# Kernel tuning notes

Measured on AMD Instinct MI355X. Metric: run time of the kernel, lower is better.

## Reference

```python
import jax, jax.numpy as jnp
import numpy as np

EMBED_DIM = 1024
NUM_HEADS = 16
HEAD_DIM = EMBED_DIM // NUM_HEADS
SCALE = HEAD_DIM ** -0.5
B, S = 2, 2048


def setup_inputs() -> dict:
    key = jax.random.key(0)
    ks = jax.random.split(key, 11)
    lim = 1.0 / np.sqrt(EMBED_DIM)
    def lin(kw, kb):
        W = jax.random.uniform(kw, (EMBED_DIM, EMBED_DIM), jnp.float32, -lim, lim)
        b = jax.random.uniform(kb, (EMBED_DIM,), jnp.float32, -lim, lim)
        return W, b
    Wq, bq = lin(ks[0], ks[1])
    Wk, bk = lin(ks[2], ks[3])
    Wv, bv = lin(ks[4], ks[5])
    Wo, bo = lin(ks[6], ks[7])
    query = jax.random.normal(ks[8], (B, S, EMBED_DIM), jnp.float32)
    key_t = jax.random.normal(ks[9], (B, S, EMBED_DIM), jnp.float32)
    value = jax.random.normal(ks[10], (B, S, EMBED_DIM), jnp.float32)
    return {"query": query, "key": key_t, "value": value,
            "Wq": Wq, "bq": bq, "Wk": Wk, "bk": bk,
            "Wv": Wv, "bv": bv, "Wo": Wo, "bo": bo}


def reference(query, key, value, Wq, bq, Wk, bk, Wv, bv, Wo, bo):
    # 'flash' path with attn_mask=None == full softmax attention (chunking is
    # only an execution schedule; per-chunk softmax is over the full key axis).
    b, s, _ = query.shape
    def heads(x, W, bias):
        y = x @ W.T + bias                      # [b, s, E]
        return y.reshape(b, s, NUM_HEADS, HEAD_DIM).transpose(0, 2, 1, 3)  # [b, h, s, d]
    q = heads(query, Wq, bq)
    k = heads(key, Wk, bk)
    v = heads(value, Wv, bv)
    scores = jnp.einsum('bhqd,bhkd->bhqk', q, k) * SCALE
    attn = jax.nn.softmax(scores, axis=-1)
    out = jnp.einsum('bhqk,bhkd->bhqd', attn, v)
    out = out.transpose(0, 2, 1, 3).reshape(b, s, EMBED_DIM)
    return out @ Wo.T + bo
```

## Files before the change

kernel.cpp:

```cpp
#include <hip/hip_runtime.h>

typedef unsigned short u16;
typedef unsigned int u32;
typedef __attribute__((ext_vector_type(8))) __bf16 bf16x8;
typedef __attribute__((ext_vector_type(4))) float f32x4;
typedef __attribute__((ext_vector_type(4))) unsigned short u16x4;
typedef __attribute__((ext_vector_type(8))) unsigned short u16x8;
typedef __attribute__((ext_vector_type(4))) unsigned int u32x4;

#define DEV static __device__ __forceinline__

DEV void async_copy16(const void* g, void* l) {
  __builtin_amdgcn_global_load_lds((const __attribute__((address_space(1))) void*)g,
                                   (__attribute__((address_space(3))) void*)l, 16, 0, 0);
}
DEV float b2f(u16 s) { union { unsigned u; float f; } v; v.u = ((unsigned)s) << 16; return v.f; }
DEV u16 f2b(float f) {
  union { float f; unsigned u; } v; v.f = f;
  unsigned r = v.u + 0x7FFFu + ((v.u >> 16) & 1u);
  return (u16)(r >> 16);
}
DEV u32 pack2bf(float a, float b) {
  u32 ua = __float_as_uint(a) + 0x8000u;
  u32 ub = __float_as_uint(b) + 0x8000u;
  return __builtin_amdgcn_perm(ub, ua, 0x07060302u);
}

#define MFMA(a, b, c) __builtin_amdgcn_mfma_f32_16x16x32_bf16((a), (b), (c), 0, 0, 0)

__global__ void detect_dtype(const unsigned* __restrict__ q, int* __restrict__ flag) {
  const int lane = threadIdx.x;
  const unsigned w = q[lane];
  const unsigned e = (w >> 7) & 0xFFu;
  const bool inr = (e >= 100u && e <= 132u);
  const unsigned long long m = __ballot(inr);
  if (lane == 0) flag[0] = (__popcll(m) >= 48) ? 1 : 0;
}

__global__ void convert_inputs(
    const void* s0, const void* s1, const void* s2,
    const void* s3, const void* s4, const void* s5, const void* s6,
    const void* s7, const void* s8, const void* s9, const void* s10,
    u16* __restrict__ d0, u16* __restrict__ d1, u16* __restrict__ d2,
    u16* __restrict__ d3, u16* __restrict__ d4, u16* __restrict__ d5, u16* __restrict__ d6,
    float* __restrict__ e7, float* __restrict__ e8, float* __restrict__ e9, float* __restrict__ e10,
    const int* __restrict__ flag)
{
  const int bi = blockIdx.y;
  const void* src = nullptr; u16* db = nullptr; float* df = nullptr; int n = 0;
  switch (bi) {
    case 0:  src = s0;  db = d0; n = 4194304; break;
    case 1:  src = s1;  db = d1; n = 4194304; break;
    case 2:  src = s2;  db = d2; n = 4194304; break;
    case 3:  src = s3;  db = d3; n = 1048576; break;
    case 4:  src = s4;  db = d4; n = 1048576; break;
    case 5:  src = s5;  db = d5; n = 1048576; break;
    case 6:  src = s6;  db = d6; n = 1048576; break;
    case 7:  src = s7;  df = e7; n = 1024; break;
    case 8:  src = s8;  df = e8; n = 1024; break;
    case 9:  src = s9;  df = e9; n = 1024; break;
    default: src = s10; df = e10; n = 1024; break;
  }
  const int isbf = flag[0];
  const int stride = gridDim.x * 256 * 8;
  for (int i = (blockIdx.x * 256 + threadIdx.x) * 8; i < n; i += stride) {
    if (db) {
      u16x8 v;
      if (isbf) {
        v = *(const u16x8*)((const u16*)src + i);
      } else {
        const float* sf = (const float*)src;
#pragma unroll
        for (int j = 0; j < 8; ++j) v[j] = f2b(sf[i + j]);
      }
      *(u16x8*)(db + i) = v;
    } else {
#pragma unroll
      for (int j = 0; j < 8; ++j) {
        float x = isbf ? b2f(((const u16*)src)[i + j]) : ((const float*)src)[i + j];
        df[i + j] = x;
      }
    }
  }
}

__global__ void gemm_qkv(const u16* __restrict__ X0, const u16* __restrict__ X1, const u16* __restrict__ X2,
                         const u16* __restrict__ W0, const u16* __restrict__ W1, const u16* __restrict__ W2,
                         const float* __restrict__ B0, const float* __restrict__ B1, const float* __restrict__ B2,
                         u16* __restrict__ Y0, u16* __restrict__ Y1, u16* __restrict__ Y2,
                         float* __restrict__ Yf, const int* __restrict__ flag, int mode0)
{
  __shared__ __align__(16) u16 smem[17408];
  u16* As = smem;
  u16* Bs = smem + 4096;

  const int z = blockIdx.z;
  const u16* X  = (z == 0) ? X0 : ((z == 1) ? X1 : X2);
  const u16* W  = (z == 0) ? W0 : ((z == 1) ? W1 : W2);
  const float* Bi = (z == 0) ? B0 : ((z == 1) ? B1 : B2);
  u16* Y        = (z == 0) ? Y0 : ((z == 1) ? Y1 : Y2);
  const int mode = mode0 ? mode0 : z;
  const int outbf = flag[0];

  const int t = threadIdx.x, wave = t >> 6, lane = t & 63;
  const int lane15 = lane & 15, quad = lane >> 4;
  const int m0 = blockIdx.y * 128, n0 = blockIdx.x * 128;

  const u16* gA = X + (size_t)(m0 + wave * 16 + (lane >> 2)) * 1024 + (lane & 3) * 8;
  const u16* gB = W + (size_t)(n0 + wave * 16 + (lane >> 2)) * 1024 + (lane & 3) * 8;
  u16* lA = &As[wave * 16 * 32];
  u16* lB = &Bs[wave * 16 * 32];

  f32x4 acc[4][4];
#pragma unroll
  for (int i = 0; i < 4; ++i)
#pragma unroll
    for (int j = 0; j < 4; ++j) acc[i][j] = (f32x4){0.f, 0.f, 0.f, 0.f};

  const int wr = wave >> 1, wc = wave & 1;

  for (int k0 = 0; k0 < 1024; k0 += 32) {
    async_copy16(gA, lA);
    async_copy16(gA + 64 * 1024, lA + 64 * 32);
    async_copy16(gB, lB);
    async_copy16(gB + 64 * 1024, lB + 64 * 32);
    gA += 32; gB += 32;
    __syncthreads();

    bf16x8 af[4], bfv[4];
#pragma unroll
    for (int mt = 0; mt < 4; ++mt)
      af[mt] = *(const bf16x8*)&As[(wr * 64 + mt * 16 + lane15) * 32 + quad * 8];
#pragma unroll
    for (int nt = 0; nt < 4; ++nt)
      bfv[nt] = *(const bf16x8*)&Bs[(wc * 64 + nt * 16 + lane15) * 32 + quad * 8];
#pragma unroll
    for (int mt = 0; mt < 4; ++mt)
#pragma unroll
      for (int nt = 0; nt < 4; ++nt)
        acc[mt][nt] = MFMA(af[mt], bfv[nt], acc[mt][nt]);
    __syncthreads();
  }

  const float qscale = 0.125f * 1.44269504088896340736f;

  if (mode == 2) {
    u16* T2 = smem;
    __syncthreads();
#pragma unroll
    for (int mt = 0; mt < 4; ++mt) {
      const int sl_base = wr * 64 + mt * 16 + quad * 4;
#pragma unroll
      for (int nt = 0; nt < 4; ++nt) {
        const int nn = wc * 64 + nt * 16 + lane15;
        const float bias_v = Bi[n0 + nn];
#pragma unroll
        for (int r = 0; r < 4; ++r) {
          const int sl = sl_base + r;
          const int sp = ((sl & 15) << 3) | (sl >> 4);
          T2[nn * 136 + sp] = f2b(acc[mt][nt][r] + bias_v);
        }
      }
    }
    __syncthreads();
    const size_t grow0 = (size_t)(m0 >> 11) * 1024 + n0;
    const int col0 = m0 & 2047;
#pragma unroll
    for (int i = 0; i < 8; ++i) {
      const int id = i * 256 + t;
      const int row = id >> 4, ch = id & 15;
      *(u16x8*)&Y[(grow0 + row) * 2048 + col0 + ch * 8] = *(const u16x8*)&T2[row * 136 + ch * 8];
    }
    return;
  }

#pragma unroll
  for (int mt = 0; mt < 4; ++mt) {
    const int m_base = m0 + wr * 64 + mt * 16 + quad * 4;
#pragma unroll
    for (int nt = 0; nt < 4; ++nt) {
      const int n = n0 + wc * 64 + nt * 16 + lane15;
      const float bias_v = Bi[n];
#pragma unroll
      for (int r = 0; r < 4; ++r) {
        const int m = m_base + r;
        float v = acc[mt][nt][r] + bias_v;
        if (mode == 0) v *= qscale;
        if (mode == 3) {
          if (outbf) Y[(size_t)m * 1024 + n] = f2b(v);
          else       Yf[(size_t)m * 1024 + n] = v;
        } else {
          size_t addr = (((size_t)(m >> 11) * 16 + (n >> 6)) * 2048 + (size_t)(m & 2047)) * 64 + (n & 63);
          Y[addr] = f2b(v);
        }
      }
    }
  }
}

__global__ __launch_bounds__(256, 2) void flash_attn(const u16* __restrict__ Qs, const u16* __restrict__ Ks,
                                                     const u16* __restrict__ Vt, u16* __restrict__ AO)
{
  __shared__ __align__(16) u16 smem[32768];
  u16* Kt = smem;
  u16* Vs = smem + 8192;

  const int t = threadIdx.x, wave = t >> 6, lane = t & 63;
  const int lane15 = lane & 15, quad = lane >> 4;
  const int l7 = lane15 & 7;
  const int bh = blockIdx.y;
  const int q0 = blockIdx.x * 128;
  u16* Pw = smem + 16384 + wave * 4096;

  const u16* Qb = Qs + ((size_t)bh * 2048 + q0) * 64;
  const u16* Kb = Ks + (size_t)bh * 2048 * 64;
  const u16* Vb = Vt + (size_t)bh * 64 * 2048;

  const int krow = lane >> 3;
  const int kchunk = (lane & 7) ^ (krow & 7);
  const int vrow = lane >> 4;
  const int vchunk = (lane & 15) ^ (((wave & 1) << 2) + vrow);

#pragma unroll
  for (int r = 0; r < 4; ++r)
    async_copy16(Qb + (size_t)(r * 32 + wave * 8 + krow) * 64 + kchunk * 8,
                 &Kt[(r * 32 + wave * 8) * 64]);
  __syncthreads();
  bf16x8 aq[2][2];
#pragma unroll
  for (int mt = 0; mt < 2; ++mt)
#pragma unroll
    for (int ks = 0; ks < 2; ++ks)
      aq[mt][ks] = *(const bf16x8*)&Kt[(wave * 32 + mt * 16 + lane15) * 64 + ((ks * 4 + quad) ^ l7) * 8];
  __syncthreads();

  f32x4 acc_o[2][4], acc_l[2];
#pragma unroll
  for (int mt = 0; mt < 2; ++mt) {
    acc_l[mt] = (f32x4){0.f, 0.f, 0.f, 0.f};
#pragma unroll
    for (int i = 0; i < 4; ++i) acc_o[mt][i] = (f32x4){0.f, 0.f, 0.f, 0.f};
  }

  u16x8 ou;
#pragma unroll
  for (int j = 0; j < 8; ++j) ou[j] = 0x3F80;
  const bf16x8 ones = __builtin_bit_cast(bf16x8, ou);

  for (int kt = 0; kt < 16; ++kt) {
#pragma unroll
    for (int r = 0; r < 4; ++r)
      async_copy16(Kb + (size_t)(kt * 128 + r * 32 + wave * 8 + krow) * 64 + kchunk * 8,
                   &Kt[(r * 32 + wave * 8) * 64]);
#pragma unroll
    for (int r = 0; r < 4; ++r)
      async_copy16(Vb + (size_t)(r * 16 + wave * 4 + vrow) * 2048 + kt * 128 + vchunk * 8,
                   &Vs[(r * 16 + wave * 4) * 128]);
    __syncthreads();

    f32x4 s[2][8];
#pragma unroll
    for (int mt = 0; mt < 2; ++mt)
#pragma unroll
      for (int nt = 0; nt < 8; ++nt) s[mt][nt] = (f32x4){0.f, 0.f, 0.f, 0.f};
#pragma unroll
    for (int ks = 0; ks < 2; ++ks) {
      bf16x8 bk[8];
#pragma unroll
      for (int nt = 0; nt < 8; ++nt)
        bk[nt] = *(const bf16x8*)&Kt[(nt * 16 + lane15) * 64 + ((ks * 4 + quad) ^ l7) * 8];
#pragma unroll
      for (int mt = 0; mt < 2; ++mt)
#pragma unroll
        for (int nt = 0; nt < 8; ++nt)
          s[mt][nt] = MFMA(aq[mt][ks], bk[nt], s[mt][nt]);
    }

#pragma unroll
    for (int mt = 0; mt < 2; ++mt)
#pragma unroll
      for (int rg = 0; rg < 4; ++rg) {
        u32x4 w;
#pragma unroll
        for (int j = 0; j < 4; ++j)
          w[j] = pack2bf(__builtin_amdgcn_exp2f(s[mt][2 * j][rg]),
                         __builtin_amdgcn_exp2f(s[mt][2 * j + 1][rg]));
        const int r = mt * 16 + quad * 4 + rg;
        *(u32x4*)&Pw[r * 128 + (lane15 ^ (r & 7)) * 8] = w;
      }
    __threadfence_block();

#pragma unroll
    for (int ks2 = 0; ks2 < 4; ++ks2) {
      bf16x8 bv[4], ap[2];
#pragma unroll
      for (int dt = 0; dt < 4; ++dt)
        bv[dt] = *(const bf16x8*)&Vs[(dt * 16 + lane15) * 128 + ((ks2 * 4 + quad) ^ l7) * 8];
#pragma unroll
      for (int mt = 0; mt < 2; ++mt)
        ap[mt] = *(const bf16x8*)&Pw[(mt * 16 + lane15) * 128 + ((ks2 * 4 + quad) ^ l7) * 8];
#pragma unroll
      for (int mt = 0; mt < 2; ++mt) {
#pragma unroll
        for (int dt = 0; dt < 4; ++dt)
          acc_o[mt][dt] = MFMA(ap[mt], bv[dt], acc_o[mt][dt]);
        acc_l[mt] = MFMA(ap[mt], ones, acc_l[mt]);
      }
    }
    __syncthreads();
  }

  float rinv[2][4];
#pragma unroll
  for (int mt = 0; mt < 2; ++mt)
#pragma unroll
    for (int rg = 0; rg < 4; ++rg) rinv[mt][rg] = 1.0f / acc_l[mt][rg];

  u16* T = smem;
#pragma unroll
  for (int mt = 0; mt < 2; ++mt)
#pragma unroll
    for (int dt = 0; dt < 4; ++dt)
#pragma unroll
      for (int rg = 0; rg < 4; ++rg)
        T[(wave * 32 + mt * 16 + quad * 4 + rg) * 72 + dt * 16 + lane15] =
            f2b(acc_o[mt][dt][rg] * rinv[mt][rg]);
  __syncthreads();

  const int b = bh >> 4, h = bh & 15;
#pragma unroll
  for (int i = 0; i < 4; ++i) {
    const int id = i * 256 + t;
    const int row = id >> 3, ch = id & 7;
    *(u16x8*)&AO[((size_t)b * 2048 + q0 + row) * 1024 + h * 64 + ch * 8] =
        *(const u16x8*)&T[row * 72 + ch * 8];
  }
}

extern "C" void kernel_launch(void* const* d_in, const int* in_sizes, int n_in,
                              void* d_out, int out_size, void* d_ws, size_t ws_size,
                              hipStream_t stream)
{
  const void* query = d_in[0];
  const void* key_  = d_in[1];
  const void* value = d_in[2];
  const void* Wq = d_in[3]; const void* bq = d_in[4];
  const void* Wk = d_in[5]; const void* bk = d_in[6];
  const void* Wv = d_in[7]; const void* bv = d_in[8];
  const void* Wo = d_in[9]; const void* bo = d_in[10];

  u16* ws = (u16*)d_ws;
  u16* Qs  = ws;
  u16* Ks  = Qs + 4194304;
  u16* Vt  = Ks + 4194304;
  u16* AO  = Vt + 4194304;
  u16* Xq  = AO + 4194304;
  u16* Xk  = Xq + 4194304;
  u16* Xv  = Xk + 4194304;
  u16* Wqc = Xv + 4194304;
  u16* Wkc = Wqc + 1048576;
  u16* Wvc = Wkc + 1048576;
  u16* Woc = Wvc + 1048576;
  float* Bc = (float*)(Woc + 1048576);
  int* flag = (int*)(Bc + 4096);

  detect_dtype<<<1, 64, 0, stream>>>((const unsigned*)query, flag);
  convert_inputs<<<dim3(128, 11), 256, 0, stream>>>(
      query, key_, value, Wq, Wk, Wv, Wo, bq, bk, bv, bo,
      Xq, Xk, Xv, Wqc, Wkc, Wvc, Woc,
      Bc, Bc + 1024, Bc + 2048, Bc + 3072, flag);

  gemm_qkv<<<dim3(8, 32, 3), 256, 0, stream>>>(Xq, Xk, Xv, Wqc, Wkc, Wvc,
                                               Bc, Bc + 1024, Bc + 2048,
                                               Qs, Ks, Vt, nullptr, flag, 0);
  flash_attn<<<dim3(16, 32), 256, 0, stream>>>(Qs, Ks, Vt, AO);
  gemm_qkv<<<dim3(8, 32, 1), 256, 0, stream>>>(AO, AO, AO, Woc, Woc, Woc,
                                               Bc + 3072, Bc + 3072, Bc + 3072,
                                               (u16*)d_out, (u16*)d_out, (u16*)d_out,
                                               (float*)d_out, flag, 3);
}
```

Baseline: 231.5 us.

## Deepen GEMM K-tile, enlarge per-wave attention tiles, inline dtype detection

Removes the separate dtype-detection kernel by detecting bf16 inputs inside convert_inputs and the output GEMM, which saves one launch. The GEMM now stages a 64-wide K slab with an XOR-swizzled LDS layout and uses launch bounds of 3, so it synchronizes half as often. The attention kernel moves to 128 threads where each wave owns 64 query rows, and it interleaves QK MFMAs with exp/pack per column pair. Larger per-wave tiles increase register pressure, and the halved block size may reduce occupancy.

```diff
diff --git a/kernel.cpp b/kernel.cpp
--- a/kernel.cpp
+++ b/kernel.cpp
@@ -4,7 +4,6 @@
 typedef unsigned int u32;
 typedef __attribute__((ext_vector_type(8))) __bf16 bf16x8;
 typedef __attribute__((ext_vector_type(4))) float f32x4;
-typedef __attribute__((ext_vector_type(4))) unsigned short u16x4;
 typedef __attribute__((ext_vector_type(8))) unsigned short u16x8;
 typedef __attribute__((ext_vector_type(4))) unsigned int u32x4;
 
@@ -25,17 +24,14 @@
   u32 ub = __float_as_uint(b) + 0x8000u;
   return __builtin_amdgcn_perm(ub, ua, 0x07060302u);
 }
-
-#define MFMA(a, b, c) __builtin_amdgcn_mfma_f32_16x16x32_bf16((a), (b), (c), 0, 0, 0)
-
-__global__ void detect_dtype(const unsigned* __restrict__ q, int* __restrict__ flag) {
-  const int lane = threadIdx.x;
-  const unsigned w = q[lane];
+DEV int wave_detect_bf16(const unsigned* q, int lane) {
+  const unsigned w = q[lane & 63];
   const unsigned e = (w >> 7) & 0xFFu;
   const bool inr = (e >= 100u && e <= 132u);
-  const unsigned long long m = __ballot(inr);
-  if (lane == 0) flag[0] = (__popcll(m) >= 48) ? 1 : 0;
-}
+  return (__popcll(__ballot(inr)) >= 48) ? 1 : 0;
+}
+
+#define MFMA(a, b, c) __builtin_amdgcn_mfma_f32_16x16x32_bf16((a), (b), (c), 0, 0, 0)
 
 __global__ void convert_inputs(
     const void* s0, const void* s1, const void* s2,
@@ -43,8 +39,7 @@
     const void* s7, const void* s8, const void* s9, const void* s10,
     u16* __restrict__ d0, u16* __restrict__ d1, u16* __restrict__ d2,
     u16* __restrict__ d3, u16* __restrict__ d4, u16* __restrict__ d5, u16* __restrict__ d6,
-    float* __restrict__ e7, float* __restrict__ e8, float* __restrict__ e9, float* __restrict__ e10,
-    const int* __restrict__ flag)
+    float* __restrict__ e7, float* __restrict__ e8, float* __restrict__ e9, float* __restrict__ e10)
 {
   const int bi = blockIdx.y;
   const void* src = nullptr; u16* db = nullptr; float* df = nullptr; int n = 0;
@@ -61,7 +56,7 @@
     case 9:  src = s9;  df = e9; n = 1024; break;
     default: src = s10; df = e10; n = 1024; break;
   }
-  const int isbf = flag[0];
+  const int isbf = wave_detect_bf16((const unsigned*)s0, threadIdx.x);
   const int stride = gridDim.x * 256 * 8;
   for (int i = (blockIdx.x * 256 + threadIdx.x) * 8; i < n; i += stride) {
     if (db) {
@@ -84,15 +79,16 @@
   }
 }
 
-__global__ void gemm_qkv(const u16* __restrict__ X0, const u16* __restrict__ X1, const u16* __restrict__ X2,
-                         const u16* __restrict__ W0, const u16* __restrict__ W1, const u16* __restrict__ W2,
-                         const float* __restrict__ B0, const float* __restrict__ B1, const float* __restrict__ B2,
-                         u16* __restrict__ Y0, u16* __restrict__ Y1, u16* __restrict__ Y2,
-                         float* __restrict__ Yf, const int* __restrict__ flag, int mode0)
+__global__ __launch_bounds__(256, 3)
+void gemm_qkv(const u16* __restrict__ X0, const u16* __restrict__ X1, const u16* __restrict__ X2,
+              const u16* __restrict__ W0, const u16* __restrict__ W1, const u16* __restrict__ W2,
+              const float* __restrict__ B0, const float* __restrict__ B1, const float* __restrict__ B2,
+              u16* __restrict__ Y0, u16* __restrict__ Y1, u16* __restrict__ Y2,
+              float* __restrict__ Yf, const unsigned* __restrict__ qdet, int mode0)
 {
   __shared__ __align__(16) u16 smem[17408];
   u16* As = smem;
-  u16* Bs = smem + 4096;
+  u16* Bs = smem + 8192;
 
   const int z = blockIdx.z;
   const u16* X  = (z == 0) ? X0 : ((z == 1) ? X1 : X2);
@@ -100,16 +96,17 @@
   const float* Bi = (z == 0) ? B0 : ((z == 1) ? B1 : B2);
   u16* Y        = (z == 0) ? Y0 : ((z == 1) ? Y1 : Y2);
   const int mode = mode0 ? mode0 : z;
-  const int outbf = flag[0];
 
   const int t = threadIdx.x, wave = t >> 6, lane = t & 63;
-  const int lane15 = lane & 15, quad = lane >> 4;
+  const int lane15 = lane & 15, quad = lane >> 4, l7 = lane15 & 7;
   const int m0 = blockIdx.y * 128, n0 = blockIdx.x * 128;
 
-  const u16* gA = X + (size_t)(m0 + wave * 16 + (lane >> 2)) * 1024 + (lane & 3) * 8;
-  const u16* gB = W + (size_t)(n0 + wave * 16 + (lane >> 2)) * 1024 + (lane & 3) * 8;
-  u16* lA = &As[wave * 16 * 32];
-  u16* lB = &Bs[wave * 16 * 32];
+  const int srow = lane >> 3;
+  const int schunk = (lane & 7) ^ srow;
+  const u16* gA = X + (size_t)(m0 + wave * 32 + srow) * 1024 + schunk * 8;
+  const u16* gB = W + (size_t)(n0 + wave * 32 + srow) * 1024 + schunk * 8;
+  u16* lA = &As[wave * 32 * 64];
+  u16* lB = &Bs[wave * 32 * 64];
 
   f32x4 acc[4][4];
 #pragma unroll
@@ -119,26 +116,29 @@
 
   const int wr = wave >> 1, wc = wave & 1;
 
-  for (int k0 = 0; k0 < 1024; k0 += 32) {
-    async_copy16(gA, lA);
-    async_copy16(gA + 64 * 1024, lA + 64 * 32);
-    async_copy16(gB, lB);
-    async_copy16(gB + 64 * 1024, lB + 64 * 32);
-    gA += 32; gB += 32;
-    __syncthreads();
-
-    bf16x8 af[4], bfv[4];
-#pragma unroll
-    for (int mt = 0; mt < 4; ++mt)
-      af[mt] = *(const bf16x8*)&As[(wr * 64 + mt * 16 + lane15) * 32 + quad * 8];
-#pragma unroll
-    for (int nt = 0; nt < 4; ++nt)
-      bfv[nt] = *(const bf16x8*)&Bs[(wc * 64 + nt * 16 + lane15) * 32 + quad * 8];
-#pragma unroll
-    for (int mt = 0; mt < 4; ++mt)
+  for (int k0 = 0; k0 < 1024; k0 += 64) {
+#pragma unroll
+    for (int r = 0; r < 4; ++r) async_copy16(gA + (size_t)r * 8 * 1024, lA + r * 8 * 64);
+#pragma unroll
+    for (int r = 0; r < 4; ++r) async_copy16(gB + (size_t)r * 8 * 1024, lB + r * 8 * 64);
+    gA += 64; gB += 64;
+    __syncthreads();
+
+#pragma unroll
+    for (int kk = 0; kk < 2; ++kk) {
+      bf16x8 af[4], bfv[4];
+#pragma unroll
+      for (int mt = 0; mt < 4; ++mt)
+        af[mt] = *(const bf16x8*)&As[(wr * 64 + mt * 16 + lane15) * 64 + ((kk * 4 + quad) ^ l7) * 8];
 #pragma unroll
       for (int nt = 0; nt < 4; ++nt)
-        acc[mt][nt] = MFMA(af[mt], bfv[nt], acc[mt][nt]);
+        bfv[nt] = *(const bf16x8*)&Bs[(wc * 64 + nt * 16 + lane15) * 64 + ((kk * 4 + quad) ^ l7) * 8];
+#pragma unroll
+      for (int mt = 0; mt < 4; ++mt)
+#pragma unroll
+        for (int nt = 0; nt < 4; ++nt)
+          acc[mt][nt] = MFMA(af[mt], bfv[nt], acc[mt][nt]);
+    }
     __syncthreads();
   }
 
@@ -173,6 +173,8 @@
     }
     return;
   }
+
+  const int outbf = (mode == 3) ? wave_detect_bf16(qdet, lane) : 1;
 
 #pragma unroll
   for (int mt = 0; mt < 4; ++mt) {
@@ -198,45 +200,44 @@
   }
 }
 
-__global__ __launch_bounds__(256, 2) void flash_attn(const u16* __restrict__ Qs, const u16* __restrict__ Ks,
-                                                     const u16* __restrict__ Vt, u16* __restrict__ AO)
+__global__ __launch_bounds__(128, 1)
+void flash_attn(const u16* __restrict__ Qs, const u16* __restrict__ Ks,
+                const u16* __restrict__ Vt, u16* __restrict__ AO)
 {
   __shared__ __align__(16) u16 smem[32768];
   u16* Kt = smem;
   u16* Vs = smem + 8192;
 
-  const int t = threadIdx.x, wave = t >> 6, lane = t & 63;
-  const int lane15 = lane & 15, quad = lane >> 4;
-  const int l7 = lane15 & 7;
+  const int t = threadIdx.x, w = t >> 6, lane = t & 63;
+  const int lane15 = lane & 15, quad = lane >> 4, l7 = lane15 & 7;
   const int bh = blockIdx.y;
   const int q0 = blockIdx.x * 128;
-  u16* Pw = smem + 16384 + wave * 4096;
+  u16* Pw = smem + 16384 + w * 8192;
 
   const u16* Qb = Qs + ((size_t)bh * 2048 + q0) * 64;
   const u16* Kb = Ks + (size_t)bh * 2048 * 64;
   const u16* Vb = Vt + (size_t)bh * 64 * 2048;
 
   const int krow = lane >> 3;
-  const int kchunk = (lane & 7) ^ (krow & 7);
+  const int kchunk = (lane & 7) ^ krow;
   const int vrow = lane >> 4;
-  const int vchunk = (lane & 15) ^ (((wave & 1) << 2) + vrow);
-
-#pragma unroll
-  for (int r = 0; r < 4; ++r)
-    async_copy16(Qb + (size_t)(r * 32 + wave * 8 + krow) * 64 + kchunk * 8,
-                 &Kt[(r * 32 + wave * 8) * 64]);
+
+#pragma unroll
+  for (int r = 0; r < 8; ++r)
+    async_copy16(Qb + (size_t)(w * 64 + r * 8 + krow) * 64 + kchunk * 8,
+                 &Kt[(w * 64 + r * 8) * 64]);
   __syncthreads();
-  bf16x8 aq[2][2];
-#pragma unroll
-  for (int mt = 0; mt < 2; ++mt)
+  bf16x8 aq[4][2];
+#pragma unroll
+  for (int mt = 0; mt < 4; ++mt)
 #pragma unroll
     for (int ks = 0; ks < 2; ++ks)
-      aq[mt][ks] = *(const bf16x8*)&Kt[(wave * 32 + mt * 16 + lane15) * 64 + ((ks * 4 + quad) ^ l7) * 8];
+      aq[mt][ks] = *(const bf16x8*)&Kt[(w * 64 + mt * 16 + lane15) * 64 + ((ks * 4 + quad) ^ l7) * 8];
   __syncthreads();
 
-  f32x4 acc_o[2][4], acc_l[2];
-#pragma unroll
-  for (int mt = 0; mt < 2; ++mt) {
+  f32x4 acc_o[4][4], acc_l[4];
+#pragma unroll
+  for (int mt = 0; mt < 4; ++mt) {
     acc_l[mt] = (f32x4){0.f, 0.f, 0.f, 0.f};
 #pragma unroll
     for (int i = 0; i < 4; ++i) acc_o[mt][i] = (f32x4){0.f, 0.f, 0.f, 0.f};
@@ -249,58 +250,60 @@
 
   for (int kt = 0; kt < 16; ++kt) {
 #pragma unroll
-    for (int r = 0; r < 4; ++r)
-      async_copy16(Kb + (size_t)(kt * 128 + r * 32 + wave * 8 + krow) * 64 + kchunk * 8,
-                   &Kt[(r * 32 + wave * 8) * 64]);
-#pragma unroll
-    for (int r = 0; r < 4; ++r)
-      async_copy16(Vb + (size_t)(r * 16 + wave * 4 + vrow) * 2048 + kt * 128 + vchunk * 8,
-                   &Vs[(r * 16 + wave * 4) * 128]);
-    __syncthreads();
-
-    f32x4 s[2][8];
-#pragma unroll
-    for (int mt = 0; mt < 2; ++mt)
-#pragma unroll
-      for (int nt = 0; nt < 8; ++nt) s[mt][nt] = (f32x4){0.f, 0.f, 0.f, 0.f};
-#pragma unroll
-    for (int ks = 0; ks < 2; ++ks) {
-      bf16x8 bk[8];
-#pragma unroll
-      for (int nt = 0; nt < 8; ++nt)
-        bk[nt] = *(const bf16x8*)&Kt[(nt * 16 + lane15) * 64 + ((ks * 4 + quad) ^ l7) * 8];
-#pragma unroll
-      for (int mt = 0; mt < 2; ++mt)
-#pragma unroll
-        for (int nt = 0; nt < 8; ++nt)
-          s[mt][nt] = MFMA(aq[mt][ks], bk[nt], s[mt][nt]);
-    }
-
-#pragma unroll
-    for (int mt = 0; mt < 2; ++mt)
+    for (int r = 0; r < 8; ++r)
+      async_copy16(Kb + (size_t)(kt * 128 + w * 64 + r * 8 + krow) * 64 + kchunk * 8,
+                   &Kt[(w * 64 + r * 8) * 64]);
+#pragma unroll
+    for (int r = 0; r < 8; ++r) {
+      const int d = w * 32 + r * 4 + vrow;
+      const int vchunk = (lane & 15) ^ (d & 7);
+      async_copy16(Vb + (size_t)d * 2048 + kt * 128 + vchunk * 8,
+                   &Vs[(w * 32 + r * 4) * 128]);
+    }
+    __syncthreads();
+
+    u32x4 wp[4][4];
+#pragma unroll
+    for (int np = 0; np < 4; ++np) {
+      bf16x8 bk[2][2];
+#pragma unroll
+      for (int sb = 0; sb < 2; ++sb)
+#pragma unroll
+        for (int ks = 0; ks < 2; ++ks)
+          bk[sb][ks] = *(const bf16x8*)&Kt[((np * 2 + sb) * 16 + lane15) * 64 + ((ks * 4 + quad) ^ l7) * 8];
+#pragma unroll
+      for (int mt = 0; mt < 4; ++mt) {
+        f32x4 s0 = (f32x4){0.f, 0.f, 0.f, 0.f}, s1 = (f32x4){0.f, 0.f, 0.f, 0.f};
+        s0 = MFMA(aq[mt][0], bk[0][0], s0);
+        s1 = MFMA(aq[mt][0], bk[1][0], s1);
+        s0 = MFMA(aq[mt][1], bk[0][1], s0);
+        s1 = MFMA(aq[mt][1], bk[1][1], s1);
+#pragma unroll
+        for (int rg = 0; rg < 4; ++rg)
+          wp[mt][rg][np] = pack2bf(__builtin_amdgcn_exp2f(s0[rg]),
+                                   __builtin_amdgcn_exp2f(s1[rg]));
+      }
+    }
+#pragma unroll
+    for (int mt = 0; mt < 4; ++mt)
 #pragma unroll
       for (int rg = 0; rg < 4; ++rg) {
-        u32x4 w;
-#pragma unroll
-        for (int j = 0; j < 4; ++j)
-          w[j] = pack2bf(__builtin_amdgcn_exp2f(s[mt][2 * j][rg]),
-                         __builtin_amdgcn_exp2f(s[mt][2 * j + 1][rg]));
         const int r = mt * 16 + quad * 4 + rg;
-        *(u32x4*)&Pw[r * 128 + (lane15 ^ (r & 7)) * 8] = w;
+        *(u32x4*)&Pw[r * 128 + (lane15 ^ (r & 7)) * 8] = wp[mt][rg];
       }
     __threadfence_block();
 
 #pragma unroll
     for (int ks2 = 0; ks2 < 4; ++ks2) {
-      bf16x8 bv[4], ap[2];
+      bf16x8 bv[4], ap[4];
 #pragma unroll
       for (int dt = 0; dt < 4; ++dt)
         bv[dt] = *(const bf16x8*)&Vs[(dt * 16 + lane15) * 128 + ((ks2 * 4 + quad) ^ l7) * 8];
 #pragma unroll
-      for (int mt = 0; mt < 2; ++mt)
+      for (int mt = 0; mt < 4; ++mt)
         ap[mt] = *(const bf16x8*)&Pw[(mt * 16 + lane15) * 128 + ((ks2 * 4 + quad) ^ l7) * 8];
 #pragma unroll
-      for (int mt = 0; mt < 2; ++mt) {
+      for (int mt = 0; mt < 4; ++mt) {
 #pragma unroll
         for (int dt = 0; dt < 4; ++dt)
           acc_o[mt][dt] = MFMA(ap[mt], bv[dt], acc_o[mt][dt]);
@@ -310,27 +313,27 @@
     __syncthreads();
   }
 
-  float rinv[2][4];
-#pragma unroll
-  for (int mt = 0; mt < 2; ++mt)
+  float rinv[4][4];
+#pragma unroll
+  for (int mt = 0; mt < 4; ++mt)
 #pragma unroll
     for (int rg = 0; rg < 4; ++rg) rinv[mt][rg] = 1.0f / acc_l[mt][rg];
 
   u16* T = smem;
 #pragma unroll
-  for (int mt = 0; mt < 2; ++mt)
+  for (int mt = 0; mt < 4; ++mt)
 #pragma unroll
     for (int dt = 0; dt < 4; ++dt)
 #pragma unroll
       for (int rg = 0; rg < 4; ++rg)
-        T[(wave * 32 + mt * 16 + quad * 4 + rg) * 72 + dt * 16 + lane15] =
+        T[(w * 64 + mt * 16 + quad * 4 + rg) * 72 + dt * 16 + lane15] =
             f2b(acc_o[mt][dt][rg] * rinv[mt][rg]);
   __syncthreads();
 
   const int b = bh >> 4, h = bh & 15;
 #pragma unroll
-  for (int i = 0; i < 4; ++i) {
-    const int id = i * 256 + t;
+  for (int i = 0; i < 8; ++i) {
+    const int id = i * 128 + t;
     const int row = id >> 3, ch = id & 7;
     *(u16x8*)&AO[((size_t)b * 2048 + q0 + row) * 1024 + h * 64 + ch * 8] =
         *(const u16x8*)&T[row * 72 + ch * 8];
@@ -362,20 +365,19 @@
   u16* Wvc = Wkc + 1048576;
   u16* Woc = Wvc + 1048576;
   float* Bc = (float*)(Woc + 1048576);
-  int* flag = (int*)(Bc + 4096);
-
-  detect_dtype<<<1, 64, 0, stream>>>((const unsigned*)query, flag);
+
   convert_inputs<<<dim3(128, 11), 256, 0, stream>>>(
       query, key_, value, Wq, Wk, Wv, Wo, bq, bk, bv, bo,
       Xq, Xk, Xv, Wqc, Wkc, Wvc, Woc,
-      Bc, Bc + 1024, Bc + 2048, Bc + 3072, flag);
+      Bc, Bc + 1024, Bc + 2048, Bc + 3072);
 
   gemm_qkv<<<dim3(8, 32, 3), 256, 0, stream>>>(Xq, Xk, Xv, Wqc, Wkc, Wvc,
                                                Bc, Bc + 1024, Bc + 2048,
-                                               Qs, Ks, Vt, nullptr, flag, 0);
-  flash_attn<<<dim3(16, 32), 256, 0, stream>>>(Qs, Ks, Vt, AO);
+                                               Qs, Ks, Vt, nullptr,
+                                               (const unsigned*)query, 0);
+  flash_attn<<<dim3(16, 32), 128, 0, stream>>>(Qs, Ks, Vt, AO);
   gemm_qkv<<<dim3(8, 32, 1), 256, 0, stream>>>(AO, AO, AO, Woc, Woc, Woc,
                                                Bc + 3072, Bc + 3072, Bc + 3072,
                                                (u16*)d_out, (u16*)d_out, (u16*)d_out,
-                                               (float*)d_out, flag, 3);
-}
+                                               (float*)d_out, (const unsigned*)query, 3);
+}
```

Result: slower. 241.4 us (+4.3%).
